# Kernel optimization log

Measured on AMD Instinct MI355X. Metric: run time of the kernel, lower is better.

The kernel has to match this reference:

```python
import jax, jax.numpy as jnp
import numpy as np

R_CUT = 5.0  # Bessel/sinc RBF cutoff (DimeNet-style e_rbf)
N_CHANNELS = 64
N_NEIGH = 1_000_000
DIM = 3


def setup_inputs() -> dict:
    key = jax.random.key(0)
    k1, k2, k3 = jax.random.split(key, 3)
    h = jax.random.normal(k1, (N_NEIGH, N_CHANNELS), dtype=jnp.float32)
    rel_poss = jax.random.normal(k2, (DIM, N_NEIGH), dtype=jnp.float32)
    W = jax.random.normal(k3, (N_CHANNELS, N_CHANNELS), dtype=jnp.float32) / jnp.sqrt(jnp.float32(N_CHANNELS))
    return {"h": h, "rel_poss": rel_poss, "W": W}


def e_rbf(r, n):
    # sinc-like radial Bessel basis: sqrt(2/c) * sin(n*pi*r/c) / r
    return jnp.sqrt(2.0 / R_CUT) * jnp.sin(n * jnp.pi * r / R_CUT) / r


def reference(h, rel_poss, W):
    # h: (a, k)  rel_poss: (x, a) with x=dim, a=n_neighbours, k=n_channels
    dists = jnp.linalg.norm(rel_poss, axis=0)            # (a,)
    nrp = rel_poss / dists                               # (x, a) unit vectors
    h = h @ W.T                                          # Linear(k_tilde->k), no bias
    n_vals = jnp.arange(1, N_CHANNELS + 1, dtype=jnp.float32)[:, None]  # (k, 1)
    radial = e_rbf(dists[None, :], n_vals)               # (k, a)
    w = radial * h.T                                     # (k, a) = radial_emb[k,a]*h[a,k]
    # A[k,x,y,z] = sum_a w[k,a] * nrp[x,a]*nrp[y,a]*nrp[z,a]  (c_out = 3)
    A = jnp.einsum('ka,xa,ya,za->kxyz', w, nrp, nrp, nrp)
    return A
```

## Files before the change

### kernel.cpp

```cpp
#include <hip/hip_runtime.h>
#include <math.h>

#define NCH 64

typedef __bf16 bf16x8 __attribute__((ext_vector_type(8)));
typedef float f32x4 __attribute__((ext_vector_type(4)));

__global__ void ab_zero(float* __restrict__ ws) {
    int i = blockIdx.x * blockDim.x + threadIdx.x;
    if (i < NCH * 10) ws[i] = 0.0f;
}

__device__ __forceinline__ void glds16(const void* g, void* l) {
    __builtin_amdgcn_global_load_lds(
        (const __attribute__((address_space(1))) void*)g,
        (__attribute__((address_space(3))) void*)l, 16, 0, 0);
}

__global__ __launch_bounds__(256, 2) void ab_main(
    const float* __restrict__ h, const float* __restrict__ rp,
    const float* __restrict__ W, float* __restrict__ ws, int N)
{
    const int lane = threadIdx.x & 63;
    const int wid  = threadIdx.x >> 6;
    const int c = lane & 15;
    const int g = lane >> 4;
    const int gwave = blockIdx.x * 4 + wid;
    const int nwave = gridDim.x * 4;

    __shared__ char  ldsb[4][2][4096];
    __shared__ float Ds[4][NCH * 10];

    bf16x8 Bf[4][2];
#pragma unroll
    for (int t = 0; t < 4; ++t)
#pragma unroll
      for (int jb = 0; jb < 2; ++jb) {
        const float* wp = W + (t * 16 + c) * NCH + jb * 32 + g * 8;
        f32x4 w0 = *(const f32x4*)wp;
        f32x4 w1 = *(const f32x4*)(wp + 4);
#pragma unroll
        for (int e = 0; e < 4; ++e) { Bf[t][jb][e] = (__bf16)w0[e]; Bf[t][jb][4 + e] = (__bf16)w1[e]; }
      }

    int offr[4];
    {
        int a0 = c * 256 + g * 32;
        int xr = (c & 7) << 4;
        offr[0] = (a0 + 0)   ^ xr;
        offr[1] = (a0 + 16)  ^ xr;
        offr[2] = (a0 + 128) ^ xr;
        offr[3] = (a0 + 144) ^ xr;
    }
    int offs[4];
#pragma unroll
    for (int k = 0; k < 4; ++k) {
        int lin = k * 1024 + lane * 16;
        int row = lin >> 8;
        offs[k] = lin ^ ((row & 7) << 4);
    }

    const int cp = (c < 10) ? c : 9;
    const int E1[10] = {0,0,0,0,0,0,1,1,1,2};
    const int E2[10] = {0,0,0,1,1,2,1,1,2,2};
    const int E3[10] = {0,1,2,1,2,2,1,2,2,2};
    const int e1 = E1[cp], e2 = E2[cp], e3 = E3[cp];

    f32x4 d2[4];
#pragma unroll
    for (int t = 0; t < 4; ++t) d2[t] = (f32x4){0.f, 0.f, 0.f, 0.f};

    const float C0 = 0.632455532033676f;
    const float cf1 = (float)(c + 1);
    const int numTiles = N >> 4;

    f32x4 Prx, Pry, Prz;
    auto stage = [&](char* dst, int tile) {
        const char* gb = (const char*)h + (size_t)tile * 4096;
#pragma unroll
        for (int k = 0; k < 4; ++k) glds16(gb + offs[k], dst + k * 1024);
    };
    auto rpload = [&](int tile) {
        const int ai = (tile << 4) + g * 4;
        Prx = *(const f32x4*)(rp + ai);
        Pry = *(const f32x4*)(rp + N + ai);
        Prz = *(const f32x4*)(rp + 2 * N + ai);
    };

    int pbuf = 0;
    if (gwave < numTiles) { stage(&ldsb[wid][0][0], gwave); rpload(gwave); }

    for (int tile = gwave; tile < numTiles; tile += nwave) {
        char* cur = &ldsb[wid][pbuf][0];
        char* nxt = &ldsb[wid][pbuf ^ 1][0];

        f32x4 h00 = *(const f32x4*)(cur + offr[0]);
        f32x4 h01 = *(const f32x4*)(cur + offr[1]);
        f32x4 h10 = *(const f32x4*)(cur + offr[2]);
        f32x4 h11 = *(const f32x4*)(cur + offr[3]);
        f32x4 px = Prx, py = Pry, pz = Prz;

        const int nt = tile + nwave;
        const int st = (nt < numTiles) ? nt : gwave;
        stage(nxt, st);
        rpload(st);

        bf16x8 Af[2];
#pragma unroll
        for (int e = 0; e < 4; ++e) {
            Af[0][e] = (__bf16)h00[e]; Af[0][4 + e] = (__bf16)h01[e];
            Af[1][e] = (__bf16)h10[e]; Af[1][4 + e] = (__bf16)h11[e];
        }

        f32x4 acc[4];
#pragma unroll
        for (int t = 0; t < 4; ++t) acc[t] = (f32x4){0.f, 0.f, 0.f, 0.f};
#pragma unroll
        for (int jb = 0; jb < 2; ++jb)
#pragma unroll
          for (int t = 0; t < 4; ++t)
            acc[t] = __builtin_amdgcn_mfma_f32_16x16x32_bf16(Af[jb], Bf[t][jb], acc[t], 0, 0, 0);

        float vm[4][4];
        bf16x8 B2;
#pragma unroll
        for (int e = 4; e < 8; ++e) B2[e] = (__bf16)0.0f;
#pragma unroll
        for (int i = 0; i < 4; ++i) {
            float x = px[i], y = py[i], z = pz[i];
            float r2 = x * x + y * y + z * z;
            float inv = rsqrtf(r2);
            float nx = x * inv, ny = y * inv, nz = z * inv;
            float rev1 = (r2 * inv) * 0.1f;
            float coef = C0 * inv;
            float s1 = (e1 == 0) ? nx : ((e1 == 1) ? ny : nz);
            float s2 = (e2 == 0) ? nx : ((e2 == 1) ? ny : nz);
            float s3 = (e3 == 0) ? nx : ((e3 == 1) ? ny : nz);
            B2[i] = (__bf16)(s1 * s2 * s3);
            float revn = cf1 * rev1;
            float rev16 = 16.0f * rev1;
#pragma unroll
            for (int t = 0; t < 4; ++t) {
                float rv = revn - floorf(revn);
                vm[t][i] = __builtin_amdgcn_sinf(rv) * coef;
                revn += rev16;
            }
        }
#pragma unroll
        for (int t = 0; t < 4; ++t) {
            bf16x8 A2;
#pragma unroll
            for (int i = 0; i < 4; ++i) A2[i] = (__bf16)(vm[t][i] * acc[t][i]);
#pragma unroll
            for (int e = 4; e < 8; ++e) A2[e] = (__bf16)0.0f;
            d2[t] = __builtin_amdgcn_mfma_f32_16x16x32_bf16(A2, B2, d2[t], 0, 0, 0);
        }
        pbuf ^= 1;
    }

    if (c < 10) {
#pragma unroll
        for (int t = 0; t < 4; ++t)
#pragma unroll
          for (int r = 0; r < 4; ++r)
            Ds[wid][(16 * t + g * 4 + r) * 10 + c] = d2[t][r];
    }
    __syncthreads();
    for (int idx = threadIdx.x; idx < NCH * 10; idx += blockDim.x) {
        float s = Ds[0][idx] + Ds[1][idx] + Ds[2][idx] + Ds[3][idx];
        atomicAdd(&ws[idx], s);
    }
}

__global__ void ab_expand(const float* __restrict__ ws, float* __restrict__ out) {
    const unsigned char tab[27] = { 0,1,2, 1,3,4, 2,4,5,
                                    1,3,4, 3,6,7, 4,7,8,
                                    2,4,5, 4,7,8, 5,8,9 };
    int i = blockIdx.x * blockDim.x + threadIdx.x;
    if (i < NCH * 27) {
        int k = i / 27, cc = i % 27;
        out[i] = ws[k * 10 + tab[cc]];
    }
}

extern "C" void kernel_launch(void* const* d_in, const int* in_sizes, int n_in,
                              void* d_out, int out_size, void* d_ws, size_t ws_size,
                              hipStream_t stream) {
    const float* h  = (const float*)d_in[0];
    const float* rp = (const float*)d_in[1];
    const float* W  = (const float*)d_in[2];
    float* out = (float*)d_out;
    float* ws  = (float*)d_ws;
    const int N = in_sizes[1] / 3;

    ab_zero<<<1, 640, 0, stream>>>(ws);
    ab_main<<<512, 256, 0, stream>>>(h, rp, W, ws, N);
    ab_expand<<<(NCH * 27 + 255) / 256, 256, 0, stream>>>(ws, out);
}
```

Before: 60.43 us.

## Triple-buffer LDS tile pipeline and fold expand kernel into last-block epilogue

Moves the per-wave h staging from double to triple buffering. A manually unrolled three-phase loop uses inline ds_read with fixed offsets and an explicit vmcnt wait, so two tiles stay in flight. The separate expand kernel is removed: a completion counter in the workspace lets the last block read the accumulated sums and write the expanded output, which saves one kernel launch. The costs are 50% more LDS per block, which may limit occupancy, hand-written waitcnt assumptions that are fragile, and a serialized tail in the final block.

```diff
diff --git a/kernel.cpp b/kernel.cpp
--- a/kernel.cpp
+++ b/kernel.cpp
@@ -8,7 +8,7 @@
 
 __global__ void ab_zero(float* __restrict__ ws) {
     int i = blockIdx.x * blockDim.x + threadIdx.x;
-    if (i < NCH * 10) ws[i] = 0.0f;
+    if (i < NCH * 10 + 1) ws[i] = 0.0f;
 }
 
 __device__ __forceinline__ void glds16(const void* g, void* l) {
@@ -19,7 +19,8 @@
 
 __global__ __launch_bounds__(256, 2) void ab_main(
     const float* __restrict__ h, const float* __restrict__ rp,
-    const float* __restrict__ W, float* __restrict__ ws, int N)
+    const float* __restrict__ W, float* __restrict__ ws,
+    float* __restrict__ out, int N)
 {
     const int lane = threadIdx.x & 63;
     const int wid  = threadIdx.x >> 6;
@@ -28,8 +29,9 @@
     const int gwave = blockIdx.x * 4 + wid;
     const int nwave = gridDim.x * 4;
 
-    __shared__ char  ldsb[4][2][4096];
+    __shared__ char  ldsb[4][3][4096];
     __shared__ float Ds[4][NCH * 10];
+    __shared__ int lastFlag;
 
     bf16x8 Bf[4][2];
 #pragma unroll
@@ -43,14 +45,16 @@
         for (int e = 0; e < 4; ++e) { Bf[t][jb][e] = (__bf16)w0[e]; Bf[t][jb][4 + e] = (__bf16)w1[e]; }
       }
 
-    int offr[4];
+    unsigned a0r, a1r, a2r, a3r;
     {
         int a0 = c * 256 + g * 32;
         int xr = (c & 7) << 4;
-        offr[0] = (a0 + 0)   ^ xr;
-        offr[1] = (a0 + 16)  ^ xr;
-        offr[2] = (a0 + 128) ^ xr;
-        offr[3] = (a0 + 144) ^ xr;
+        auto p = (__attribute__((address_space(3))) char*)&ldsb[wid][0][0];
+        unsigned base = (unsigned)(size_t)p;
+        a0r = base + ((a0 + 0)   ^ xr);
+        a1r = base + ((a0 + 16)  ^ xr);
+        a2r = base + ((a0 + 128) ^ xr);
+        a3r = base + ((a0 + 144) ^ xr);
     }
     int offs[4];
 #pragma unroll
@@ -74,44 +78,21 @@
     const float cf1 = (float)(c + 1);
     const int numTiles = N >> 4;
 
-    f32x4 Prx, Pry, Prz;
-    auto stage = [&](char* dst, int tile) {
+    auto stage = [&](int buf, int tile) {
         const char* gb = (const char*)h + (size_t)tile * 4096;
+        char* dst = &ldsb[wid][buf][0];
 #pragma unroll
         for (int k = 0; k < 4; ++k) glds16(gb + offs[k], dst + k * 1024);
     };
-    auto rpload = [&](int tile) {
-        const int ai = (tile << 4) + g * 4;
-        Prx = *(const f32x4*)(rp + ai);
-        Pry = *(const f32x4*)(rp + N + ai);
-        Prz = *(const f32x4*)(rp + 2 * N + ai);
-    };
-
-    int pbuf = 0;
-    if (gwave < numTiles) { stage(&ldsb[wid][0][0], gwave); rpload(gwave); }
-
-    for (int tile = gwave; tile < numTiles; tile += nwave) {
-        char* cur = &ldsb[wid][pbuf][0];
-        char* nxt = &ldsb[wid][pbuf ^ 1][0];
-
-        f32x4 h00 = *(const f32x4*)(cur + offr[0]);
-        f32x4 h01 = *(const f32x4*)(cur + offr[1]);
-        f32x4 h10 = *(const f32x4*)(cur + offr[2]);
-        f32x4 h11 = *(const f32x4*)(cur + offr[3]);
-        f32x4 px = Prx, py = Pry, pz = Prz;
-
-        const int nt = tile + nwave;
-        const int st = (nt < numTiles) ? nt : gwave;
-        stage(nxt, st);
-        rpload(st);
-
+
+    auto computeTile = [&](f32x4 h00, f32x4 h01, f32x4 h10, f32x4 h11,
+                           f32x4 px, f32x4 py, f32x4 pz) {
         bf16x8 Af[2];
 #pragma unroll
         for (int e = 0; e < 4; ++e) {
             Af[0][e] = (__bf16)h00[e]; Af[0][4 + e] = (__bf16)h01[e];
             Af[1][e] = (__bf16)h10[e]; Af[1][4 + e] = (__bf16)h11[e];
         }
-
         f32x4 acc[4];
 #pragma unroll
         for (int t = 0; t < 4; ++t) acc[t] = (f32x4){0.f, 0.f, 0.f, 0.f};
@@ -155,8 +136,52 @@
             for (int e = 4; e < 8; ++e) A2[e] = (__bf16)0.0f;
             d2[t] = __builtin_amdgcn_mfma_f32_16x16x32_bf16(A2, B2, d2[t], 0, 0, 0);
         }
-        pbuf ^= 1;
-    }
+    };
+
+    f32x4 Apx, Apy, Apz, Bpx, Bpy, Bpz, Cpx, Cpy, Cpz;
+
+#define RPLOAD(P, t) do {                                   \
+        const int ai_ = ((t) << 4) + g * 4;                 \
+        P##px = *(const f32x4*)(rp + ai_);                  \
+        P##py = *(const f32x4*)(rp + N + ai_);              \
+        P##pz = *(const f32x4*)(rp + 2 * N + ai_);          \
+    } while (0)
+
+#define BODY(OFFSTR, STBUF, RPC, RPF, T) do {                               \
+        asm volatile("s_waitcnt vmcnt(7)" ::: "memory");                    \
+        f32x4 h00_, h01_, h10_, h11_;                                       \
+        asm volatile("ds_read_b128 %0, %1 " OFFSTR : "=&v"(h00_) : "v"(a0r)); \
+        asm volatile("ds_read_b128 %0, %1 " OFFSTR : "=&v"(h01_) : "v"(a1r)); \
+        asm volatile("ds_read_b128 %0, %1 " OFFSTR : "=&v"(h10_) : "v"(a2r)); \
+        asm volatile("ds_read_b128 %0, %1 " OFFSTR : "=&v"(h11_) : "v"(a3r)); \
+        f32x4 px_ = RPC##px, py_ = RPC##py, pz_ = RPC##pz;                  \
+        { int tn_ = (T) + 2 * nwave;                                        \
+          int st_ = (tn_ < numTiles) ? tn_ : gwave;                         \
+          stage(STBUF, st_); RPLOAD(RPF, st_); }                            \
+        asm volatile("s_waitcnt lgkmcnt(0)" ::: "memory");                  \
+        __builtin_amdgcn_sched_barrier(0);                                  \
+        computeTile(h00_, h01_, h10_, h11_, px_, py_, pz_);                 \
+    } while (0)
+
+    int tile = gwave;
+    if (tile < numTiles) {
+        stage(0, tile); RPLOAD(A, tile);
+        {
+            int t1 = tile + nwave;
+            int t1c = (t1 < numTiles) ? t1 : tile;
+            stage(1, t1c); RPLOAD(B, t1c);
+        }
+        for (;;) {
+            BODY("offset:0",    2, A, C, tile);
+            tile += nwave; if (tile >= numTiles) break;
+            BODY("offset:4096", 0, B, A, tile);
+            tile += nwave; if (tile >= numTiles) break;
+            BODY("offset:8192", 1, C, B, tile);
+            tile += nwave; if (tile >= numTiles) break;
+        }
+    }
+#undef BODY
+#undef RPLOAD
 
     if (c < 10) {
 #pragma unroll
@@ -170,16 +195,24 @@
         float s = Ds[0][idx] + Ds[1][idx] + Ds[2][idx] + Ds[3][idx];
         atomicAdd(&ws[idx], s);
     }
-}
-
-__global__ void ab_expand(const float* __restrict__ ws, float* __restrict__ out) {
-    const unsigned char tab[27] = { 0,1,2, 1,3,4, 2,4,5,
-                                    1,3,4, 3,6,7, 4,7,8,
-                                    2,4,5, 4,7,8, 5,8,9 };
-    int i = blockIdx.x * blockDim.x + threadIdx.x;
-    if (i < NCH * 27) {
-        int k = i / 27, cc = i % 27;
-        out[i] = ws[k * 10 + tab[cc]];
+    __threadfence();
+    if (threadIdx.x == 0) {
+        unsigned old = atomicAdd((unsigned*)&ws[NCH * 10], 1u);
+        lastFlag = (old == gridDim.x - 1) ? 1 : 0;
+    }
+    __syncthreads();
+    if (lastFlag) {
+        for (int idx = threadIdx.x; idx < NCH * 10; idx += blockDim.x)
+            Ds[0][idx] = __hip_atomic_load(&ws[idx], __ATOMIC_RELAXED,
+                                           __HIP_MEMORY_SCOPE_AGENT);
+        __syncthreads();
+        const unsigned char tab[27] = { 0,1,2, 1,3,4, 2,4,5,
+                                        1,3,4, 3,6,7, 4,7,8,
+                                        2,4,5, 4,7,8, 5,8,9 };
+        for (int i = threadIdx.x; i < NCH * 27; i += blockDim.x) {
+            int k = i / 27, cc = i % 27;
+            out[i] = Ds[0][k * 10 + tab[cc]];
+        }
     }
 }
 
@@ -193,7 +226,6 @@
     float* ws  = (float*)d_ws;
     const int N = in_sizes[1] / 3;
 
-    ab_zero<<<1, 640, 0, stream>>>(ws);
-    ab_main<<<512, 256, 0, stream>>>(h, rp, W, ws, N);
-    ab_expand<<<(NCH * 27 + 255) / 256, 256, 0, stream>>>(ws, out);
-}
+    ab_zero<<<3, 256, 0, stream>>>(ws);
+    ab_main<<<512, 256, 0, stream>>>(h, rp, W, ws, out, N);
+}
```

Measured after the change: 100.2 us. 65.9% more time.
